# Performance work log

Measured on AMD Instinct MI355X. Metric: run time of the kernel, lower is better.

The kernel has to match this reference:

```python
import jax, jax.numpy as jnp
import numpy as np

B, N, D = 32, 128, 1024


def _euclid_cost(a, b):
    # a: [N, D], b: [N, D] -> [N, N] Euclidean distances (torch.cdist p=2)
    a = a.astype(np.float64)
    b = b.astype(np.float64)
    sq = (a * a).sum(-1)[:, None] + (b * b).sum(-1)[None, :] - 2.0 * (a @ b.T)
    return np.sqrt(np.maximum(sq, 0.0))


def _hungarian(cost):
    """Exact LAP via shortest augmenting path (Kuhn-Munkres with potentials).
    Returns col_for_row: row i is matched to column col_for_row[i].
    Equivalent to scipy.optimize.linear_sum_assignment on a square matrix
    (row_ind == arange(N))."""
    n = cost.shape[0]
    INF = 1e18
    c = cost.astype(np.float64)
    u = np.zeros(n + 1)
    v = np.zeros(n + 1)
    p = np.zeros(n + 1, dtype=np.int64)   # p[j] = row matched to column j (1-based)
    way = np.zeros(n + 1, dtype=np.int64)
    for i in range(1, n + 1):
        p[0] = i
        j0 = 0
        minv = np.full(n + 1, INF)
        used = np.zeros(n + 1, dtype=bool)
        while True:
            used[j0] = True
            i0 = p[j0]
            free = ~used[1:]
            cand = c[i0 - 1] - u[i0] - v[1:]
            better = free & (cand < minv[1:])
            idx = np.nonzero(better)[0]
            minv[idx + 1] = cand[idx]
            way[idx + 1] = j0
            free_j = np.nonzero(free)[0] + 1
            j1 = free_j[np.argmin(minv[free_j])]
            delta = minv[j1]
            u[p[used]] += delta
            v[used] -= delta
            minv[~used] -= delta
            j0 = j1
            if p[j0] == 0:
                break
        while j0:
            j1 = way[j0]
            p[j0] = p[j1]
            j0 = j1
    col_for_row = np.zeros(n, dtype=np.int64)
    for j in range(1, n + 1):
        col_for_row[p[j] - 1] = j - 1
    return col_for_row


def _match(pred_nodes, target_nodes):
    # Host-side exact bipartite matching (mirrors the .cpu() + scipy solve;
    # non-differentiable, indices treated as constants like torch's detach()).
    pn = np.asarray(jax.device_get(pred_nodes))
    tn = np.asarray(jax.device_get(target_nodes))
    cols = [_hungarian(_euclid_cost(pn[b], tn[b])) for b in range(pn.shape[0])]
    return jnp.asarray(np.stack(cols))  # [B, N] int64


def setup_inputs() -> dict:
    key = jax.random.key(0)
    k1, k2, k3, k4 = jax.random.split(key, 4)
    return {
        "pred_nodes": jax.random.normal(k1, (B, N, D), dtype=jnp.float32),
        "target_nodes": jax.random.normal(k2, (B, N, D), dtype=jnp.float32),
        "pred_adj": jax.random.normal(k3, (B, N, N), dtype=jnp.float32),
        "target_adj": jax.random.normal(k4, (B, N, N), dtype=jnp.float32),
    }


def reference(pred_nodes, target_nodes, pred_adj, target_adj):
    col = _match(pred_nodes, target_nodes)  # [B, N]; row_ind is identity
    # matched target nodes: target_nodes[b][col_ind]
    tn_m = jnp.take_along_axis(target_nodes, col[:, :, None], axis=1)  # [B, N, D]
    # nn.MSELoss() = mean over elements per sample; losses summed over batch
    node_loss = jnp.mean((pred_nodes - tn_m) ** 2, axis=(1, 2)).sum()
    # target_adj[b][col_ind][:, col_ind]; pred_adj row_ind gather is identity
    ta_m = jnp.take_along_axis(target_adj, col[:, :, None], axis=1)
    ta_m = jnp.take_along_axis(ta_m, col[:, None, :], axis=2)  # [B, N, N]
    edge_loss = jnp.mean((pred_adj - ta_m) ** 2, axis=(1, 2)).sum()
    return node_loss, edge_loss
```

## Files before the change

### kernel.cpp

```cpp
#include <hip/hip_runtime.h>
#include <hip/hip_bf16.h>
#include <math.h>

#define BB 32
#define NN 128
#define DD 1024
#define INF64 1e30

__global__ __launch_bounds__(128) void cost_kernel(const float* __restrict__ pred,
                                                   const float* __restrict__ tgt,
                                                   double* __restrict__ cost) {
  extern __shared__ double a_s[];
  __shared__ double na_s[8];
  int blk = blockIdx.x;
  int b = blk >> 4;
  int it = (blk & 15) << 3;
  const float* Ab = pred + ((size_t)b * NN + it) * DD;
  const float* Bb = tgt + (size_t)b * NN * DD;
  for (int t = threadIdx.x; t < 8 * DD / 4; t += 128) {
    float4 v = ((const float4*)Ab)[t];
    double2* d = (double2*)&a_s[(size_t)t * 4];
    d[0] = double2{(double)v.x, (double)v.y};
    d[1] = double2{(double)v.z, (double)v.w};
  }
  __syncthreads();
  if (threadIdx.x < 8) {
    const double* ar = a_s + (size_t)threadIdx.x * DD;
    double s0 = 0, s1 = 0, s2 = 0, s3 = 0;
    for (int k = 0; k < DD; k += 4) {
      s0 += ar[k] * ar[k];
      s1 += ar[k + 1] * ar[k + 1];
      s2 += ar[k + 2] * ar[k + 2];
      s3 += ar[k + 3] * ar[k + 3];
    }
    na_s[threadIdx.x] = (s0 + s1) + (s2 + s3);
  }
  __syncthreads();
  const int j = threadIdx.x;
  const float4* brow = (const float4*)(Bb + (size_t)j * DD);
  double acc[8];
#pragma unroll
  for (int r = 0; r < 8; r++) acc[r] = 0.0;
  double nb = 0.0;
  for (int k4 = 0; k4 < DD / 4; k4++) {
    float4 bv = brow[k4];
    double b0 = (double)bv.x, b1 = (double)bv.y, b2 = (double)bv.z, b3 = (double)bv.w;
    nb += b0 * b0 + b1 * b1 + b2 * b2 + b3 * b3;
    const double* ar = a_s + (size_t)k4 * 4;
#pragma unroll
    for (int r = 0; r < 8; r++) {
      const double* a = ar + (size_t)r * DD;
      acc[r] += a[0] * b0 + a[1] * b1 + a[2] * b2 + a[3] * b3;
    }
  }
#pragma unroll
  for (int r = 0; r < 8; r++) {
    double sq = na_s[r] + nb - 2.0 * acc[r];
    cost[(((size_t)b * NN) + it + r) * NN + j] = sqrt(fmax(sq, 0.0));
  }
}

union f64u { double d; unsigned int i[2]; };

__device__ __forceinline__ double readlane_f64(double x, int lane) {
  f64u u; u.d = x;
  f64u v;
  v.i[0] = (unsigned)__builtin_amdgcn_readlane((int)u.i[0], lane);
  v.i[1] = (unsigned)__builtin_amdgcn_readlane((int)u.i[1], lane);
  return v.d;
}

__device__ __forceinline__ double readpair_f64(double a, double b, int idx) {
  int l = (idx - 1) & 63;
  double ra = readlane_f64(a, l);
  double rb = readlane_f64(b, l);
  return ((idx - 1) >> 6) ? rb : ra;
}

__device__ __forceinline__ int readpair_i32(int a, int b, int idx) {
  int l = (idx - 1) & 63;
  int ra = __builtin_amdgcn_readlane(a, l);
  int rb = __builtin_amdgcn_readlane(b, l);
  return ((idx - 1) >> 6) ? rb : ra;
}

__device__ __forceinline__ double pack_key(double m, int idx) {
  unsigned long long bits = __double_as_longlong(fmax(m, 0.0));
  bits = (bits & ~127ull) | (unsigned long long)idx;
  return __longlong_as_double(bits);
}

#define DPP_MIN_STEP(r, CTRL)                                                        \
  do {                                                                               \
    f64u _t; _t.d = (r);                                                             \
    f64u _s;                                                                         \
    _s.i[0] = (unsigned)__builtin_amdgcn_update_dpp((int)_t.i[0], (int)_t.i[0],      \
                                                    (CTRL), 0xF, 0xF, false);        \
    _s.i[1] = (unsigned)__builtin_amdgcn_update_dpp((int)_t.i[1], (int)_t.i[1],      \
                                                    (CTRL), 0xF, 0xF, false);        \
    (r) = fmin((r), _s.d);                                                           \
  } while (0)

#define DPP_MIN_CHAIN(r)          \
  do {                            \
    DPP_MIN_STEP(r, 0x111);       \
    DPP_MIN_STEP(r, 0x112);       \
    DPP_MIN_STEP(r, 0x114);       \
    DPP_MIN_STEP(r, 0x118);       \
    DPP_MIN_STEP(r, 0x142);       \
    DPP_MIN_STEP(r, 0x143);       \
  } while (0)

__global__ __launch_bounds__(64) void hungarian_kernel(const double* __restrict__ cost,
                                                       int* __restrict__ colfor) {
  extern __shared__ double lds[];
  const int b = blockIdx.x;
  const double* C = cost + (size_t)b * NN * NN;
  const int lane = threadIdx.x;
  const int jA = lane + 1;
  const int jB = lane + 65;

  {
    double2* dst = (double2*)lds;
#pragma unroll 4
    for (int i = 0; i < NN; i++) {
      double gA = C[(size_t)i * NN + lane];
      double gB = C[(size_t)i * NN + lane + 64];
      dst[i * 64 + lane] = double2{gA, gB};
    }
  }
  __syncthreads();

  double vA = INF64, vB = INF64;
  int argA = 0, argB = 0;
#pragma unroll 4
  for (int i = 0; i < NN; i++) {
    double2 cc = ((const double2*)lds)[i * 64 + lane];
    if (cc.x < vA) { vA = cc.x; argA = i + 1; }
    if (cc.y < vB) { vB = cc.y; argB = i + 1; }
  }

  unsigned long long asgLo = 0ull, asgHi = 0ull;
  int pA = 0, pB = 0;
  for (int j = 1; j <= NN; j++) {
    int ar = readpair_i32(argA, argB, j);
    bool freeRow = (ar <= 64) ? !((asgLo >> (ar - 1)) & 1ull)
                              : !((asgHi >> (ar - 65)) & 1ull);
    if (freeRow) {
      if (ar <= 64) asgLo |= 1ull << (ar - 1); else asgHi |= 1ull << (ar - 65);
      if (j == jA) pA = ar;
      if (j == jB) pB = ar;
    }
  }

  unsigned long long freeLo = __ballot(pA == 0);
  unsigned long long freeHi = __ballot(pB == 0);

  double uA = 0.0, uB = 0.0;
  unsigned long long mLo = ~asgLo, mHi = ~asgHi;

  while ((mLo | mHi) != 0ull) {
    int i = mLo ? (__builtin_ctzll(mLo) + 1) : (__builtin_ctzll(mHi) + 65);
    if (i <= 64) mLo &= ~(1ull << (i - 1)); else mHi &= ~(1ull << (i - 65));

    double minvA = INF64, minvB = INF64;
    int wayA = 0, wayB = 0;
    int usedA = 0, usedB = 0;
    unsigned long long usedRowLo = 0ull, usedRowHi = 0ull;
    int j0 = 0;
    int i0 = i;
    while (true) {
      usedA |= (j0 == jA);
      usedB |= (j0 == jB);
      if (i0 <= 64) usedRowLo |= 1ull << (i0 - 1); else usedRowHi |= 1ull << (i0 - 65);
      double u_i0 = readpair_f64(uA, uB, i0);
      double2 cc = ((const double2*)lds)[(i0 - 1) * 64 + lane];
      double candA = cc.x - u_i0 - vA;
      double candB = cc.y - u_i0 - vB;
      if (!usedA && candA < minvA) { minvA = candA; wayA = j0; }
      if (!usedB && candB < minvB) { minvB = candB; wayB = j0; }
      double kA = pack_key(usedA ? INF64 : minvA, lane);
      double kB = pack_key(usedB ? INF64 : minvB, lane + 64);
      double r = fmin(kA, kB);
      DPP_MIN_CHAIN(r);
      double rmin = readlane_f64(r, 63);
      unsigned long long bits = __double_as_longlong(rmin);
      int j1 = (int)(bits & 127ull) + 1;
      double delta = __longlong_as_double((long long)(bits & ~127ull));
      if ((usedRowLo >> lane) & 1ull) uA += delta;
      if ((usedRowHi >> lane) & 1ull) uB += delta;
      if (usedA) vA -= delta; else minvA -= delta;
      if (usedB) vB -= delta; else minvB -= delta;
      bool isFree = (j1 <= 64) ? ((freeLo >> (j1 - 1)) & 1ull)
                               : ((freeHi >> (j1 - 65)) & 1ull);
      j0 = j1;
      if (isFree) break;
      i0 = readpair_i32(pA, pB, j1);
    }
    int jfin = j0;
    int j = jfin;
    while (j) {
      int wj = readpair_i32(wayA, wayB, j);
      int pn = (wj == 0) ? i : readpair_i32(pA, pB, wj);
      if (j == jA) pA = pn;
      if (j == jB) pB = pn;
      j = wj;
    }
    if (jfin <= 64) freeLo &= ~(1ull << (jfin - 1));
    else            freeHi &= ~(1ull << (jfin - 65));
  }
  colfor[b * NN + (pA - 1)] = jA - 1;
  colfor[b * NN + (pB - 1)] = jB - 1;
}

__global__ __launch_bounds__(256) void node_loss_kernel(const float* __restrict__ pred,
                                                        const float* __restrict__ tgt,
                                                        const int* __restrict__ col,
                                                        double* __restrict__ partial) {
  const size_t total = (size_t)BB * NN * (DD / 4);
  double s = 0.0;
  for (size_t idx = (size_t)blockIdx.x * blockDim.x + threadIdx.x; idx < total;
       idx += (size_t)gridDim.x * blockDim.x) {
    size_t k4 = idx & (DD / 4 - 1);
    size_t bi = idx / (DD / 4);
    int i = (int)(bi & (NN - 1));
    int b = (int)(bi >> 7);
    int c = col[b * NN + i];
    float4 pv = ((const float4*)pred)[idx];
    float4 tv = ((const float4*)(tgt + ((size_t)b * NN + c) * DD))[k4];
    float d0 = pv.x - tv.x, d1 = pv.y - tv.y, d2 = pv.z - tv.z, d3 = pv.w - tv.w;
    s += (double)d0 * d0 + (double)d1 * d1 + (double)d2 * d2 + (double)d3 * d3;
  }
  __shared__ double red[256];
  red[threadIdx.x] = s;
  __syncthreads();
  for (int off = 128; off > 0; off >>= 1) {
    if (threadIdx.x < off) red[threadIdx.x] += red[threadIdx.x + off];
    __syncthreads();
  }
  if (threadIdx.x == 0) partial[blockIdx.x] = red[0];
}

__global__ __launch_bounds__(256) void edge_loss_kernel(const float* __restrict__ padj,
                                                        const float* __restrict__ tadj,
                                                        const int* __restrict__ col,
                                                        double* __restrict__ partial) {
  const size_t total = (size_t)BB * NN * NN;
  double s = 0.0;
  for (size_t idx = (size_t)blockIdx.x * blockDim.x + threadIdx.x; idx < total;
       idx += (size_t)gridDim.x * blockDim.x) {
    int j = (int)(idx & (NN - 1));
    size_t bi = idx >> 7;
    int i = (int)(bi & (NN - 1));
    int b = (int)(bi >> 7);
    int ci = col[b * NN + i];
    int cj = col[b * NN + j];
    float diff = padj[idx] - tadj[((size_t)b * NN + ci) * NN + cj];
    s += (double)diff * (double)diff;
  }
  __shared__ double red[256];
  red[threadIdx.x] = s;
  __syncthreads();
  for (int off = 128; off > 0; off >>= 1) {
    if (threadIdx.x < off) red[threadIdx.x] += red[threadIdx.x + off];
    __syncthreads();
  }
  if (threadIdx.x == 0) partial[blockIdx.x] = red[0];
}

__global__ __launch_bounds__(256) void finalize_kernel(const double* __restrict__ nodeP, int nNode,
                                                       const double* __restrict__ edgeP, int nEdge,
                                                       float* __restrict__ out) {
  __shared__ double red[256];
  double s = 0.0;
  for (int t = threadIdx.x; t < nNode; t += 256) s += nodeP[t];
  red[threadIdx.x] = s;
  __syncthreads();
  for (int off = 128; off > 0; off >>= 1) {
    if (threadIdx.x < off) red[threadIdx.x] += red[threadIdx.x + off];
    __syncthreads();
  }
  double nodeSum = red[0];
  __syncthreads();
  s = 0.0;
  for (int t = threadIdx.x; t < nEdge; t += 256) s += edgeP[t];
  red[threadIdx.x] = s;
  __syncthreads();
  for (int off = 128; off > 0; off >>= 1) {
    if (threadIdx.x < off) red[threadIdx.x] += red[threadIdx.x + off];
    __syncthreads();
  }
  if (threadIdx.x == 0) {
    out[0] = (float)(nodeSum / (double)(NN * DD));
    out[1] = (float)(red[0] / (double)(NN * NN));
  }
}

extern "C" void kernel_launch(void* const* d_in, const int* in_sizes, int n_in,
                              void* d_out, int out_size, void* d_ws, size_t ws_size,
                              hipStream_t stream) {
  const float* pred_nodes   = (const float*)d_in[0];
  const float* target_nodes = (const float*)d_in[1];
  const float* pred_adj     = (const float*)d_in[2];
  const float* target_adj   = (const float*)d_in[3];
  float* out = (float*)d_out;

  char* ws = (char*)d_ws;
  double* cost = (double*)ws;
  size_t off = (size_t)BB * NN * NN * sizeof(double);
  int* col = (int*)(ws + off);
  off += (size_t)BB * NN * sizeof(int);
  double* nodeP = (double*)(ws + off);
  double* edgeP = nodeP + 512;

  cost_kernel<<<BB * 16, 128, 65536, stream>>>(pred_nodes, target_nodes, cost);
  hungarian_kernel<<<BB, 64, 131072, stream>>>(cost, col);
  node_loss_kernel<<<512, 256, 0, stream>>>(pred_nodes, target_nodes, col, nodeP);
  edge_loss_kernel<<<128, 256, 0, stream>>>(pred_adj, target_adj, col, edgeP);
  finalize_kernel<<<1, 256, 0, stream>>>(nodeP, 512, edgeP, 128, out);
}
```

Before: 946.8 us.

## Warm-start Hungarian duals for greedy matches and shrink cost kernel LDS

The Hungarian kernel now derives row potentials and column potentials for the rows that the greedy column-min pass already matched, so those rows start from a feasible dual state. The intent is to make the later augmenting-path searches shorter. The LDS cost copy becomes a flat row-major copy, and the next-row lookup is moved earlier in the inner loop. The cost kernel keeps the A rows as float in LDS, uses 64 threads that each compute two columns, and computes the row norms in parallel, which cuts LDS size and the float-to-double conversion work. The risk is a correctness or tie-handling change from the warm-started duals, and lower parallelism in the cost kernel.

```diff
diff --git a/kernel.cpp b/kernel.cpp
--- a/kernel.cpp
+++ b/kernel.cpp
@@ -7,56 +7,65 @@
 #define DD 1024
 #define INF64 1e30
 
-__global__ __launch_bounds__(128) void cost_kernel(const float* __restrict__ pred,
-                                                   const float* __restrict__ tgt,
-                                                   double* __restrict__ cost) {
-  extern __shared__ double a_s[];
+__global__ __launch_bounds__(64) void cost_kernel(const float* __restrict__ pred,
+                                                  const float* __restrict__ tgt,
+                                                  double* __restrict__ cost) {
+  __shared__ float a_s[8 * DD];
+  __shared__ double red_s[64];
   __shared__ double na_s[8];
   int blk = blockIdx.x;
   int b = blk >> 4;
   int it = (blk & 15) << 3;
   const float* Ab = pred + ((size_t)b * NN + it) * DD;
   const float* Bb = tgt + (size_t)b * NN * DD;
-  for (int t = threadIdx.x; t < 8 * DD / 4; t += 128) {
-    float4 v = ((const float4*)Ab)[t];
-    double2* d = (double2*)&a_s[(size_t)t * 4];
-    d[0] = double2{(double)v.x, (double)v.y};
-    d[1] = double2{(double)v.z, (double)v.w};
-  }
-  __syncthreads();
-  if (threadIdx.x < 8) {
-    const double* ar = a_s + (size_t)threadIdx.x * DD;
-    double s0 = 0, s1 = 0, s2 = 0, s3 = 0;
-    for (int k = 0; k < DD; k += 4) {
-      s0 += ar[k] * ar[k];
-      s1 += ar[k + 1] * ar[k + 1];
-      s2 += ar[k + 2] * ar[k + 2];
-      s3 += ar[k + 3] * ar[k + 3];
-    }
-    na_s[threadIdx.x] = (s0 + s1) + (s2 + s3);
-  }
-  __syncthreads();
-  const int j = threadIdx.x;
-  const float4* brow = (const float4*)(Bb + (size_t)j * DD);
-  double acc[8];
+  const int lane = threadIdx.x;
+  for (int t = lane; t < 8 * DD / 4; t += 64) {
+    ((float4*)a_s)[t] = ((const float4*)Ab)[t];
+  }
+  __syncthreads();
+  {
+    int r = lane >> 3, o = lane & 7;
+    const float* ar = a_s + (size_t)r * DD;
+    double s = 0.0;
+    for (int k = o; k < DD; k += 8) { double x = (double)ar[k]; s += x * x; }
+    red_s[lane] = s;
+  }
+  __syncthreads();
+  if (lane < 8) {
+    double s = 0.0;
 #pragma unroll
-  for (int r = 0; r < 8; r++) acc[r] = 0.0;
-  double nb = 0.0;
+    for (int m = 0; m < 8; m++) s += red_s[lane * 8 + m];
+    na_s[lane] = s;
+  }
+  __syncthreads();
+  const float4* brow0 = (const float4*)(Bb + (size_t)lane * DD);
+  const float4* brow1 = (const float4*)(Bb + (size_t)(lane + 64) * DD);
+  double acc0[8], acc1[8];
+#pragma unroll
+  for (int r = 0; r < 8; r++) { acc0[r] = 0.0; acc1[r] = 0.0; }
+  double nb0 = 0.0, nb1 = 0.0;
   for (int k4 = 0; k4 < DD / 4; k4++) {
-    float4 bv = brow[k4];
-    double b0 = (double)bv.x, b1 = (double)bv.y, b2 = (double)bv.z, b3 = (double)bv.w;
-    nb += b0 * b0 + b1 * b1 + b2 * b2 + b3 * b3;
-    const double* ar = a_s + (size_t)k4 * 4;
+    float4 b0 = brow0[k4];
+    float4 b1 = brow1[k4];
+    double d00 = (double)b0.x, d01 = (double)b0.y, d02 = (double)b0.z, d03 = (double)b0.w;
+    double d10 = (double)b1.x, d11 = (double)b1.y, d12 = (double)b1.z, d13 = (double)b1.w;
+    nb0 += d00 * d00 + d01 * d01 + d02 * d02 + d03 * d03;
+    nb1 += d10 * d10 + d11 * d11 + d12 * d12 + d13 * d13;
 #pragma unroll
     for (int r = 0; r < 8; r++) {
-      const double* a = ar + (size_t)r * DD;
-      acc[r] += a[0] * b0 + a[1] * b1 + a[2] * b2 + a[3] * b3;
+      float4 av = ((const float4*)(a_s + (size_t)r * DD))[k4];
+      double a0 = (double)av.x, a1 = (double)av.y, a2 = (double)av.z, a3 = (double)av.w;
+      acc0[r] += a0 * d00 + a1 * d01 + a2 * d02 + a3 * d03;
+      acc1[r] += a0 * d10 + a1 * d11 + a2 * d12 + a3 * d13;
     }
   }
 #pragma unroll
   for (int r = 0; r < 8; r++) {
-    double sq = na_s[r] + nb - 2.0 * acc[r];
-    cost[(((size_t)b * NN) + it + r) * NN + j] = sqrt(fmax(sq, 0.0));
+    double sq0 = na_s[r] + nb0 - 2.0 * acc0[r];
+    double sq1 = na_s[r] + nb1 - 2.0 * acc1[r];
+    size_t base = (((size_t)b * NN) + it + r) * NN;
+    cost[base + lane] = sqrt(fmax(sq0, 0.0));
+    cost[base + lane + 64] = sqrt(fmax(sq1, 0.0));
   }
 }
 
@@ -121,13 +130,10 @@
   const int jB = lane + 65;
 
   {
+    const double2* src = (const double2*)C;
     double2* dst = (double2*)lds;
-#pragma unroll 4
-    for (int i = 0; i < NN; i++) {
-      double gA = C[(size_t)i * NN + lane];
-      double gB = C[(size_t)i * NN + lane + 64];
-      dst[i * 64 + lane] = double2{gA, gB};
-    }
+#pragma unroll 8
+    for (int t = lane; t < NN * NN / 2; t += 64) dst[t] = src[t];
   }
   __syncthreads();
 
@@ -135,28 +141,50 @@
   int argA = 0, argB = 0;
 #pragma unroll 4
   for (int i = 0; i < NN; i++) {
-    double2 cc = ((const double2*)lds)[i * 64 + lane];
-    if (cc.x < vA) { vA = cc.x; argA = i + 1; }
-    if (cc.y < vB) { vB = cc.y; argB = i + 1; }
+    double cA = lds[(size_t)i * NN + lane];
+    double cB = lds[(size_t)i * NN + lane + 64];
+    if (cA < vA) { vA = cA; argA = i + 1; }
+    if (cB < vB) { vB = cB; argB = i + 1; }
   }
 
   unsigned long long asgLo = 0ull, asgHi = 0ull;
   int pA = 0, pB = 0;
+  int rowColA = 0, rowColB = 0;
   for (int j = 1; j <= NN; j++) {
     int ar = readpair_i32(argA, argB, j);
     bool freeRow = (ar <= 64) ? !((asgLo >> (ar - 1)) & 1ull)
                               : !((asgHi >> (ar - 65)) & 1ull);
     if (freeRow) {
-      if (ar <= 64) asgLo |= 1ull << (ar - 1); else asgHi |= 1ull << (ar - 65);
+      if (ar <= 64) { asgLo |= 1ull << (ar - 1); if (lane == ar - 1) rowColA = j; }
+      else          { asgHi |= 1ull << (ar - 65); if (lane == ar - 65) rowColB = j; }
       if (j == jA) pA = ar;
       if (j == jB) pB = ar;
     }
   }
 
+  double uA = 0.0, uB = 0.0;
+
+  for (int i = 1; i <= NN; i++) {
+    bool matched = (i <= 64) ? ((asgLo >> (i - 1)) & 1ull)
+                             : ((asgHi >> (i - 65)) & 1ull);
+    if (!matched) continue;
+    int j1 = readpair_i32(rowColA, rowColB, i);
+    double cA = lds[(size_t)(i - 1) * NN + lane];
+    double cB = lds[(size_t)(i - 1) * NN + lane + 64];
+    double sA = (jA == j1) ? INF64 : cA - vA;
+    double sB = (jB == j1) ? INF64 : cB - vB;
+    double r = fmin(sA, sB);
+    DPP_MIN_CHAIN(r);
+    double min2 = readlane_f64(r, 63);
+    if (i <= 64) { if (lane == i - 1) uA = min2; }
+    else         { if (lane == i - 65) uB = min2; }
+    double cj1 = readpair_f64(cA, cB, j1);
+    if (jA == j1) vA = cj1 - min2;
+    if (jB == j1) vB = cj1 - min2;
+  }
+
   unsigned long long freeLo = __ballot(pA == 0);
   unsigned long long freeHi = __ballot(pB == 0);
-
-  double uA = 0.0, uB = 0.0;
   unsigned long long mLo = ~asgLo, mHi = ~asgHi;
 
   while ((mLo | mHi) != 0ull) {
@@ -174,9 +202,10 @@
       usedB |= (j0 == jB);
       if (i0 <= 64) usedRowLo |= 1ull << (i0 - 1); else usedRowHi |= 1ull << (i0 - 65);
       double u_i0 = readpair_f64(uA, uB, i0);
-      double2 cc = ((const double2*)lds)[(i0 - 1) * 64 + lane];
-      double candA = cc.x - u_i0 - vA;
-      double candB = cc.y - u_i0 - vB;
+      double cA = lds[(size_t)(i0 - 1) * NN + lane];
+      double cB = lds[(size_t)(i0 - 1) * NN + lane + 64];
+      double candA = cA - u_i0 - vA;
+      double candB = cB - u_i0 - vB;
       if (!usedA && candA < minvA) { minvA = candA; wayA = j0; }
       if (!usedB && candB < minvB) { minvB = candB; wayB = j0; }
       double kA = pack_key(usedA ? INF64 : minvA, lane);
@@ -187,15 +216,16 @@
       unsigned long long bits = __double_as_longlong(rmin);
       int j1 = (int)(bits & 127ull) + 1;
       double delta = __longlong_as_double((long long)(bits & ~127ull));
+      bool isFree = (j1 <= 64) ? ((freeLo >> (j1 - 1)) & 1ull)
+                               : ((freeHi >> (j1 - 65)) & 1ull);
+      int i0next = readpair_i32(pA, pB, j1);
       if ((usedRowLo >> lane) & 1ull) uA += delta;
       if ((usedRowHi >> lane) & 1ull) uB += delta;
       if (usedA) vA -= delta; else minvA -= delta;
       if (usedB) vB -= delta; else minvB -= delta;
-      bool isFree = (j1 <= 64) ? ((freeLo >> (j1 - 1)) & 1ull)
-                               : ((freeHi >> (j1 - 65)) & 1ull);
       j0 = j1;
       if (isFree) break;
-      i0 = readpair_i32(pA, pB, j1);
+      i0 = i0next;
     }
     int jfin = j0;
     int j = jfin;
@@ -313,7 +343,7 @@
   double* nodeP = (double*)(ws + off);
   double* edgeP = nodeP + 512;
 
-  cost_kernel<<<BB * 16, 128, 65536, stream>>>(pred_nodes, target_nodes, cost);
+  cost_kernel<<<BB * 16, 64, 0, stream>>>(pred_nodes, target_nodes, cost);
   hungarian_kernel<<<BB, 64, 131072, stream>>>(cost, col);
   node_loss_kernel<<<512, 256, 0, stream>>>(pred_nodes, target_nodes, col, nodeP);
   edge_loss_kernel<<<128, 256, 0, stream>>>(pred_adj, target_adj, col, edgeP);
```

New measurement: 903.1 us. 1.05x faster.
